# Optimization experiments

Hardware: AMD Instinct MI355X
Metric: run time of the kernel (lower is better)

## Reference

```python
import jax, jax.numpy as jnp
import numpy as np

B, L, CIN, DLOI, NPTS0, NPTS1, H = 2, 5000, 256, 128, 32, 8, 256
HALF = DLOI // 2
EPS = 1e-5


def _bn_params(k, c):
    k1, k2, k3, k4 = jax.random.split(k, 4)
    gamma = 1.0 + 0.1 * jax.random.normal(k1, (c,), jnp.float32)
    beta = 0.1 * jax.random.normal(k2, (c,), jnp.float32)
    mean = 0.1 * jax.random.normal(k3, (c,), jnp.float32)
    var = 0.5 + jax.random.uniform(k4, (c,), jnp.float32)
    return jnp.stack([gamma, beta, mean, var])  # [4, c]


def setup_inputs():
    key = jax.random.key(0)
    ks = jax.random.split(key, 12)
    feature = jax.random.normal(ks[0], (B, CIN, H, H), jnp.float32)
    lines = jax.random.uniform(ks[1], (B, L, 2, 2), jnp.float32, minval=0.0, maxval=255.0)
    w_fc1 = 0.05 * jax.random.normal(ks[2], (DLOI, CIN), jnp.float32)
    b_fc1 = jnp.zeros((DLOI,), jnp.float32)
    bn1 = _bn_params(ks[3], DLOI)
    c1_w = 0.1 * jax.random.normal(ks[4], (HALF, DLOI), jnp.float32)
    c1_b = jnp.zeros((HALF,), jnp.float32)
    bn2 = _bn_params(ks[5], HALF)
    c2_w = 0.1 * jax.random.normal(ks[6], (HALF, HALF, 3), jnp.float32)
    c2_b = jnp.zeros((HALF,), jnp.float32)
    bn3 = _bn_params(ks[7], HALF)
    c3_w = 0.1 * jax.random.normal(ks[8], (DLOI, HALF), jnp.float32)
    c3_b = jnp.zeros((DLOI,), jnp.float32)
    w_fc2 = 0.03 * jax.random.normal(ks[9], (4, DLOI * NPTS1), jnp.float32)
    b_fc2 = jnp.zeros((4,), jnp.float32)
    return {"feature": feature, "lines": lines, "w_fc1": w_fc1, "b_fc1": b_fc1,
            "bn1": bn1, "c1_w": c1_w, "c1_b": c1_b, "bn2": bn2, "c2_w": c2_w,
            "c2_b": c2_b, "bn3": bn3, "c3_w": c3_w, "c3_b": c3_b,
            "w_fc2": w_fc2, "b_fc2": b_fc2}


def _bn(v, p):
    # v: [N, C, P], p: [4, C] = gamma, beta, running_mean, running_var (eval mode)
    scale = (p[0] * jax.lax.rsqrt(p[3] + EPS))[None, :, None]
    shift = p[1][None, :, None]
    return (v - p[2][None, :, None]) * scale + shift


def _forward(feature, lines, w_fc1, b_fc1, bn1, c1_w, c1_b, bn2, c2_w, c2_b,
             bn3, c3_w, c3_b, w_fc2, b_fc2):
    # fc1: 1x1 conv over backbone feature -> [B, DLOI, H, H]
    x = jnp.einsum('bchw,oc->bohw', feature, w_fc1) + b_fc1[None, :, None, None]

    # sample NPTS0 points along each line: p = p0*lam + p1*(1-lam) - 0.5
    lam = jnp.linspace(0.0, 1.0, NPTS0, dtype=jnp.float32)[:, None]  # [NPTS0, 1]
    p = lines[:, :, 0:1, :] * lam + lines[:, :, 1:2, :] * (1.0 - lam) - 0.5  # [B,L,NPTS0,2]
    px, py = p[..., 0], p[..., 1]
    px0 = jnp.clip(jnp.floor(px), 0.0, H - 1.0)
    py0 = jnp.clip(jnp.floor(py), 0.0, H - 1.0)
    px1 = jnp.clip(px0 + 1.0, 0.0, H - 1.0)
    py1 = jnp.clip(py0 + 1.0, 0.0, H - 1.0)
    i0, j0 = px0.astype(jnp.int32), py0.astype(jnp.int32)
    i1, j1 = px1.astype(jnp.int32), py1.astype(jnp.int32)
    w00 = (px1 - px) * (py1 - py)
    w10 = (px - px0) * (py1 - py)
    w01 = (px1 - px) * (py - py0)
    w11 = (px - px0) * (py - py0)

    def gather_one(feat, i0b, j0b, i1b, j1b, a, b, c, d):
        # feat [C,H,W]; indices/weights [L, NPTS0] -> [C, L, NPTS0]
        return (feat[:, i0b, j0b] * a + feat[:, i1b, j0b] * b
                + feat[:, i0b, j1b] * c + feat[:, i1b, j1b] * d)

    xp = jax.vmap(gather_one)(x, i0, j0, i1, j1, w00, w10, w01, w11)  # [B,C,L,NPTS0]
    xp = xp.transpose(0, 2, 1, 3).reshape(B * L, DLOI, NPTS0)

    # MaxPool1d(kernel=4, stride=4): NPTS0 -> NPTS1
    xp = xp.reshape(B * L, DLOI, NPTS1, NPTS0 // NPTS1).max(-1)

    # Bottleneck1D (eval-mode BN): x + op(x)
    h = jax.nn.relu(_bn(xp, bn1))
    h = jnp.einsum('ncp,oc->nop', h, c1_w) + c1_b[None, :, None]
    h = jax.nn.relu(_bn(h, bn2))
    h = jax.lax.conv_general_dilated(h, c2_w, window_strides=(1,), padding=((1, 1),),
                                     dimension_numbers=('NCH', 'OIH', 'NCH')) + c2_b[None, :, None]
    h = jax.nn.relu(_bn(h, bn3))
    h = jnp.einsum('ncp,oc->nop', h, c3_w) + c3_b[None, :, None]
    y = xp + h

    # fc2: ReLU + Linear(DLOI*NPTS1 -> 4), then softmax scores
    flat = y.reshape(B * L, DLOI * NPTS1)
    logits = jax.nn.relu(flat) @ w_fc2.T + b_fc2
    s = jax.nn.softmax(logits, axis=-1)
    return s


def reference(feature, lines, w_fc1, b_fc1, bn1, c1_w, c1_b, bn2, c2_w, c2_b,
              bn3, c3_w, c3_b, w_fc2, b_fc2):
    return _forward(feature, lines, w_fc1, b_fc1, bn1, c1_w, c1_b, bn2, c2_w,
                    c2_b, bn3, c3_w, c3_b, w_fc2, b_fc2)
```

## Files before the change

### kernel.cpp

```cpp
#include <hip/hip_runtime.h>
#include <math.h>
#include <stdint.h>

#define HH 256
#define LPB 5000

typedef _Float16 h2v  __attribute__((ext_vector_type(2)));
typedef _Float16 f16x8 __attribute__((ext_vector_type(8)));
typedef float    f32x4 __attribute__((ext_vector_type(4)));

__device__ __forceinline__ h2v u2h(unsigned int u) { return __builtin_bit_cast(h2v, u); }
__device__ __forceinline__ unsigned int h2u(h2v h) { return __builtin_bit_cast(unsigned int, h); }

__device__ __forceinline__ float fdot2(h2v a, unsigned int w, float c) {
#if __has_builtin(__builtin_amdgcn_fdot2)
    return __builtin_amdgcn_fdot2(a, u2h(w), c, false);
#else
    h2v b = u2h(w);
    return c + (float)a[0] * (float)b[0] + (float)a[1] * (float)b[1];
#endif
}

__device__ __forceinline__ h2v relu2(h2v a) {
    h2v z = (h2v)(_Float16)0.f;
#if __has_builtin(__builtin_elementwise_max)
    return __builtin_elementwise_max(a, z);
#else
    h2v r; r[0] = a[0] > z[0] ? a[0] : z[0]; r[1] = a[1] > z[1] ? a[1] : z[1]; return r;
#endif
}
__device__ __forceinline__ h2v hmax2v(h2v a, h2v b) {
#if __has_builtin(__builtin_elementwise_max)
    return __builtin_elementwise_max(a, b);
#else
    h2v r; r[0] = a[0] > b[0] ? a[0] : b[0]; r[1] = a[1] > b[1] ? a[1] : b[1]; return r;
#endif
}

__global__ __launch_bounds__(256) void prep_small(
    const float* __restrict__ w_fc1, const float* __restrict__ c1w,
    const float* __restrict__ c2w,  const float* __restrict__ c3w,
    const float* __restrict__ wfc2, const float* __restrict__ bn1,
    const float* __restrict__ bn2,  const float* __restrict__ bn3,
    _Float16* __restrict__ wf16, _Float16* __restrict__ w1r,
    _Float16* __restrict__ w2r, _Float16* __restrict__ w3r,
    unsigned int* __restrict__ wfc2p, unsigned int* __restrict__ bn_pk)
{
    int i = blockIdx.x * 256 + threadIdx.x;
    if (i < 32768) { wf16[i] = (_Float16)w_fc1[i]; return; }
    i -= 32768;
    if (i < 8192) {
        w1r[i] = (_Float16)c1w[i]; return;
    }
    i -= 8192;
    if (i < 12288) {
        int ii = i & 63, o = (i >> 6) & 63, tap = i >> 12;
        w2r[i] = (_Float16)c2w[(o * 64 + ii) * 3 + tap]; return;
    }
    i -= 12288;
    if (i < 8192) {
        w3r[i] = (_Float16)c3w[i]; return;
    }
    i -= 8192;
    if (i < 2048) {
        int c2 = i & 63, p = (i >> 6) & 7, j = i >> 9;
        h2v v = { (_Float16)wfc2[j * 1024 + (2 * c2) * 8 + p],
                  (_Float16)wfc2[j * 1024 + (2 * c2 + 1) * 8 + p] };
        wfc2p[(j * 8 + p) * 64 + c2] = h2u(v); return;
    }
    i -= 2048;
    if (i < 128) {
        const float* bn; int C, base, hcount;
        if (i < 64)      { bn = bn1; C = 128; base = 0;   hcount = 64; }
        else if (i < 96) { bn = bn2; C = 64;  base = 128; hcount = 32; i -= 64; }
        else             { bn = bn3; C = 64;  base = 192; hcount = 32; i -= 96; }
        int c0 = 2 * i, c1 = 2 * i + 1;
        float s0 = bn[c0] * rsqrtf(bn[3 * C + c0] + 1e-5f);
        float s1 = bn[c1] * rsqrtf(bn[3 * C + c1] + 1e-5f);
        float h0 = bn[C + c0] - bn[2 * C + c0] * s0;
        float h1 = bn[C + c1] - bn[2 * C + c1] * s1;
        h2v sv = { (_Float16)s0, (_Float16)s1 };
        h2v hv = { (_Float16)h0, (_Float16)h1 };
        bn_pk[base + i] = h2u(sv);
        bn_pk[base + hcount + i] = h2u(hv);
    }
}

__global__ __launch_bounds__(256, 4) void fc1_fused(
    const float* __restrict__ feat,
    const _Float16* __restrict__ W,
    const float* __restrict__ bias,
    unsigned int* __restrict__ X)
{
    __shared__ float Tf[32 * 132];
    __shared__ _Float16 Wl[128 * 40];
    const int t = threadIdx.x;
    const int lane = t & 63, wave = t >> 6;
    const int wm = wave & 1, wn = wave >> 1;
    const int pix0g = blockIdx.x << 7;
    const int b = blockIdx.x >> 9;
    const int pix0l = pix0g & 65535;
    const float* fbase = feat + (size_t)b * (256u * 65536u) + pix0l;

    f32x4 acc[4][4];
#pragma unroll
    for (int a = 0; a < 4; a++)
#pragma unroll
        for (int c = 0; c < 4; c++) acc[a][c] = (f32x4)0.f;

    for (int ks = 0; ks < 8; ks++) {
        const int k0 = ks * 32;
        __syncthreads();
#pragma unroll
        for (int r = 0; r < 4; r++) {
            int idx = t + r * 256;
            int c = idx >> 5, p4 = idx & 31;
            float4 v = *(const float4*)(fbase + (size_t)(k0 + c) * 65536 + p4 * 4);
            *(float4*)&Tf[c * 132 + p4 * 4] = v;
        }
#pragma unroll
        for (int r = 0; r < 2; r++) {
            int idx = t + r * 256;
            int row = idx >> 2, ko = (idx & 3) * 8;
            *(uint4*)&Wl[row * 40 + ko] = *(const uint4*)(W + row * 256 + k0 + ko);
        }
        __syncthreads();
        f16x8 af[4], bf[4];
#pragma unroll
        for (int mt = 0; mt < 4; mt++)
            af[mt] = *(const f16x8*)&Wl[(wm * 64 + mt * 16 + (lane & 15)) * 40 + (lane >> 4) * 8];
#pragma unroll
        for (int nt = 0; nt < 4; nt++) {
            int q = wn * 64 + nt * 16 + (lane & 15);
            int cb = (lane >> 4) * 8;
            f16x8 v;
#pragma unroll
            for (int j = 0; j < 8; j++) v[j] = (_Float16)Tf[(cb + j) * 132 + q];
            bf[nt] = v;
        }
#pragma unroll
        for (int mt = 0; mt < 4; mt++)
#pragma unroll
            for (int nt = 0; nt < 4; nt++)
                acc[mt][nt] = __builtin_amdgcn_mfma_f32_16x16x32_f16(af[mt], bf[nt], acc[mt][nt], 0, 0, 0);
    }
#pragma unroll
    for (int mt = 0; mt < 4; mt++) {
        int o = wm * 64 + mt * 16 + (lane >> 4) * 4;
        float4 b4 = *(const float4*)(bias + o);
#pragma unroll
        for (int nt = 0; nt < 4; nt++) {
            int pix = pix0g + wn * 64 + nt * 16 + (lane & 15);
            f32x4 a = acc[mt][nt];
            h2v lo = { (_Float16)(a[0] + b4.x), (_Float16)(a[1] + b4.y) };
            h2v hi = { (_Float16)(a[2] + b4.z), (_Float16)(a[3] + b4.w) };
            uint2 v = { h2u(lo), h2u(hi) };
            *(uint2*)(X + (size_t)pix * 64 + (o >> 1)) = v;
        }
    }
}

__global__ __launch_bounds__(256, 4) void line_v5(
    const unsigned int* __restrict__ X,
    const float* __restrict__ lines,
    const _Float16* __restrict__ w1r, const float* __restrict__ c1b,
    const _Float16* __restrict__ w2r, const float* __restrict__ c2b,
    const _Float16* __restrict__ w3r, const float* __restrict__ c3b,
    const unsigned int* __restrict__ wfc2p, const float* __restrict__ bfc2,
    const unsigned int* __restrict__ bn_pk,
    float* __restrict__ out)
{
    __shared__ int geoB[256];
    __shared__ unsigned int geoWA[256], geoWB[256];
    __shared__ unsigned int xp[64 * 68];
    __shared__ unsigned int abuf[64 * 68];
    __shared__ float red[128];

    const int t = threadIdx.x;
    const int n0 = blockIdx.x * 8;
    const int lane = t & 63;
    const int w = t >> 6;
    const int l15 = lane & 15;
    const int kg = lane >> 4;
    const int ko8 = kg * 8;

    {
        int l = t >> 5, k = t & 31;
        int n = n0 + l;
        float4 ln = *(const float4*)(lines + n * 4);
        float lam = (float)k / 31.0f;
        float px = ln.x * lam + ln.z * (1.f - lam) - 0.5f;
        float py = ln.y * lam + ln.w * (1.f - lam) - 0.5f;
        float px0 = fminf(fmaxf(floorf(px), 0.f), 255.f);
        float py0 = fminf(fmaxf(floorf(py), 0.f), 255.f);
        float dx = px - px0, dy = py - py0;
        float ex = 1.f - dx, ey = 1.f - dy;
        h2v wA = { (_Float16)(ex * ey), (_Float16)(dx * ey) };
        h2v wB = { (_Float16)(ex * dy), (_Float16)(dx * dy) };
        int b = (n >= LPB) ? 1 : 0;
        int pixflat = (b << 16) + ((int)px0 << 8) + (int)py0;
        geoB[t] = pixflat << 6;
        geoWA[t] = h2u(wA); geoWB[t] = h2u(wB);
    }
    __syncthreads();

    {
        const int c8 = t & 15;
        const int sub = t >> 4;
        const int line = sub >> 1;
        const int gbase = (sub & 1) * 4;
        const uint4* xq = (const uint4*)X;
        uint4 s1 = *(const uint4*)(bn_pk + c8 * 4);
        uint4 h1 = *(const uint4*)(bn_pk + 64 + c8 * 4);
#pragma unroll
        for (int lg = 0; lg < 4; lg++) {
            int g = gbase + lg;
            int ptb = line * 32 + g * 4;
            uint4 q[4][4];
            unsigned int wAv[4], wBv[4];
#pragma unroll
            for (int s = 0; s < 4; s++) {
                int pt = ptb + s;
                int base4 = (geoB[pt] >> 2) + c8;
                wAv[s] = geoWA[pt]; wBv[s] = geoWB[pt];
                q[s][0] = xq[base4];
                q[s][1] = xq[base4 + 4096];
                q[s][2] = xq[base4 + 16];
                q[s][3] = xq[base4 + 4112];
            }
            h2v m0, m1, m2, m3;
#pragma unroll
            for (int s = 0; s < 4; s++) {
                h2v wA = u2h(wAv[s]), wB = u2h(wBv[s]);
                h2v w00 = { wA[0], wA[0] }, w10 = { wA[1], wA[1] };
                h2v w01 = { wB[0], wB[0] }, w11 = { wB[1], wB[1] };
                h2v v0 = u2h(q[s][0].x) * w00 + u2h(q[s][1].x) * w10 + u2h(q[s][2].x) * w01 + u2h(q[s][3].x) * w11;
                h2v v1 = u2h(q[s][0].y) * w00 + u2h(q[s][1].y) * w10 + u2h(q[s][2].y) * w01 + u2h(q[s][3].y) * w11;
                h2v v2 = u2h(q[s][0].z) * w00 + u2h(q[s][1].z) * w10 + u2h(q[s][2].z) * w01 + u2h(q[s][3].z) * w11;
                h2v v3 = u2h(q[s][0].w) * w00 + u2h(q[s][1].w) * w10 + u2h(q[s][2].w) * w01 + u2h(q[s][3].w) * w11;
                if (s == 0) { m0 = v0; m1 = v1; m2 = v2; m3 = v3; }
                else { m0 = hmax2v(m0, v0); m1 = hmax2v(m1, v1);
                       m2 = hmax2v(m2, v2); m3 = hmax2v(m3, v3); }
            }
            int colw = line * 8 + g;
            uint4 raw = { h2u(m0), h2u(m1), h2u(m2), h2u(m3) };
            *(uint4*)&xp[colw * 68 + c8 * 4] = raw;
            h2v r0 = relu2(m0 * u2h(s1.x) + u2h(h1.x));
            h2v r1 = relu2(m1 * u2h(s1.y) + u2h(h1.y));
            h2v r2 = relu2(m2 * u2h(s1.z) + u2h(h1.z));
            h2v r3 = relu2(m3 * u2h(s1.w) + u2h(h1.w));
            uint4 act = { h2u(r0), h2u(r1), h2u(r2), h2u(r3) };
            *(uint4*)&abuf[colw * 68 + c8 * 4] = act;
        }
    }
    __syncthreads();

    f32x4 acc1[4];
#pragma unroll
    for (int nt = 0; nt < 4; nt++) acc1[nt] = (f32x4)0.f;
    {
        const int o = w * 16 + l15;
        f16x8 af[4];
#pragma unroll
        for (int kt = 0; kt < 4; kt++)
            af[kt] = *(const f16x8*)(w1r + o * 128 + kt * 32 + ko8);
        __builtin_amdgcn_s_setprio(1);
#pragma unroll
        for (int nt = 0; nt < 4; nt++) {
            const int colb = nt * 16 + l15;
#pragma unroll
            for (int kt = 0; kt < 4; kt++) {
                f16x8 bf = *(const f16x8*)&abuf[colb * 68 + kt * 16 + kg * 4];
                acc1[nt] = __builtin_amdgcn_mfma_f32_16x16x32_f16(af[kt], bf, acc1[nt], 0, 0, 0);
            }
        }
        __builtin_amdgcn_s_setprio(0);
    }
    __syncthreads();

    {
        float4 b1 = *(const float4*)(c1b + w * 16 + kg * 4);
        const int o2 = w * 8 + kg * 2;
        h2v sA = u2h(bn_pk[128 + o2]), sB = u2h(bn_pk[128 + o2 + 1]);
        h2v hA = u2h(bn_pk[160 + o2]), hB = u2h(bn_pk[160 + o2 + 1]);
#pragma unroll
        for (int nt = 0; nt < 4; nt++) {
            const int col = nt * 16 + l15;
            const int colp = (col >> 3) * 10 + 1 + (col & 7);
            h2v v0 = { (_Float16)(acc1[nt][0] + b1.x), (_Float16)(acc1[nt][1] + b1.y) };
            h2v v1 = { (_Float16)(acc1[nt][2] + b1.z), (_Float16)(acc1[nt][3] + b1.w) };
            v0 = relu2(v0 * sA + hA);
            v1 = relu2(v1 * sB + hB);
            uint2 u = { h2u(v0), h2u(v1) };
            *(uint2*)&abuf[colp * 36 + o2] = u;
        }
#pragma unroll
        for (int e = 0; e < 2; e++) {
            int idx = t * 2 + e;
            int pc = idx >> 5, i2 = idx & 31;
            int pl = pc >> 1, side = pc & 1;
            abuf[(pl * 10 + side * 9) * 36 + i2] = 0;
        }
    }
    __syncthreads();

    f32x4 acc2[4];
#pragma unroll
    for (int nt = 0; nt < 4; nt++) acc2[nt] = (f32x4)0.f;
    {
        const int o = w * 16 + l15;
        const int colp0 = (l15 >> 3) * 10 + 1 + (l15 & 7);
        __builtin_amdgcn_s_setprio(1);
#pragma unroll
        for (int tap = 0; tap < 3; tap++) {
            f16x8 wa0 = *(const f16x8*)(w2r + (tap * 64 + o) * 64 + ko8);
            f16x8 wa1 = *(const f16x8*)(w2r + (tap * 64 + o) * 64 + 32 + ko8);
#pragma unroll
            for (int nt = 0; nt < 4; nt++) {
                const int cp = colp0 + nt * 20 + tap - 1;
                f16x8 b0 = *(const f16x8*)&abuf[cp * 36 + kg * 4];
                f16x8 b1 = *(const f16x8*)&abuf[cp * 36 + 16 + kg * 4];
                acc2[nt] = __builtin_amdgcn_mfma_f32_16x16x32_f16(wa0, b0, acc2[nt], 0, 0, 0);
                acc2[nt] = __builtin_amdgcn_mfma_f32_16x16x32_f16(wa1, b1, acc2[nt], 0, 0, 0);
            }
        }
        __builtin_amdgcn_s_setprio(0);
    }
    __syncthreads();

    {
        float4 b2 = *(const float4*)(c2b + w * 16 + kg * 4);
        const int o2 = w * 8 + kg * 2;
        h2v sA = u2h(bn_pk[192 + o2]), sB = u2h(bn_pk[192 + o2 + 1]);
        h2v hA = u2h(bn_pk[224 + o2]), hB = u2h(bn_pk[224 + o2 + 1]);
#pragma unroll
        for (int nt = 0; nt < 4; nt++) {
            const int col = nt * 16 + l15;
            h2v v0 = { (_Float16)(acc2[nt][0] + b2.x), (_Float16)(acc2[nt][1] + b2.y) };
            h2v v1 = { (_Float16)(acc2[nt][2] + b2.z), (_Float16)(acc2[nt][3] + b2.w) };
            v0 = relu2(v0 * sA + hA);
            v1 = relu2(v1 * sB + hB);
            uint2 u = { h2u(v0), h2u(v1) };
            *(uint2*)&abuf[col * 36 + o2] = u;
        }
    }
    __syncthreads();

    {
#pragma unroll
        for (int mi = 0; mi < 2; mi++) {
            const int om = (2 * w + mi) * 16 + l15;
            f16x8 af0 = *(const f16x8*)(w3r + om * 64 + ko8);
            f16x8 af1 = *(const f16x8*)(w3r + om * 64 + 32 + ko8);
            f32x4 acc3[4];
#pragma unroll
            for (int nt = 0; nt < 4; nt++) acc3[nt] = (f32x4)0.f;
            __builtin_amdgcn_s_setprio(1);
#pragma unroll
            for (int nt = 0; nt < 4; nt++) {
                const int col = nt * 16 + l15;
                f16x8 b0 = *(const f16x8*)&abuf[col * 36 + kg * 4];
                f16x8 b1 = *(const f16x8*)&abuf[col * 36 + 16 + kg * 4];
                acc3[nt] = __builtin_amdgcn_mfma_f32_16x16x32_f16(af0, b0, acc3[nt], 0, 0, 0);
                acc3[nt] = __builtin_amdgcn_mfma_f32_16x16x32_f16(af1, b1, acc3[nt], 0, 0, 0);
            }
            __builtin_amdgcn_s_setprio(0);
            float4 b3 = *(const float4*)(c3b + (2 * w + mi) * 16 + kg * 4);
            const int o2 = (2 * w + mi) * 8 + kg * 2;
#pragma unroll
            for (int nt = 0; nt < 4; nt++) {
                const int col = nt * 16 + l15;
                uint2 xv = *(const uint2*)&xp[col * 68 + o2];
                h2v y0 = { (_Float16)(acc3[nt][0] + b3.x), (_Float16)(acc3[nt][1] + b3.y) };
                h2v y1 = { (_Float16)(acc3[nt][2] + b3.z), (_Float16)(acc3[nt][3] + b3.w) };
                y0 = relu2(u2h(xv.x) + y0);
                y1 = relu2(u2h(xv.y) + y1);
                uint2 u = { h2u(y0), h2u(y1) };
                *(uint2*)&xp[col * 68 + o2] = u;
            }
        }
    }
    __syncthreads();

    {
        const int og = w;
        const int col = t & 63;
        const int obH = __builtin_amdgcn_readfirstlane(og * 16);
        const int p = col & 7, l = col >> 3;
        h2v yv[16];
#pragma unroll
        for (int j = 0; j < 16; j++) yv[j] = u2h(xp[col * 68 + obH + j]);
        float aj[4] = { 0.f, 0.f, 0.f, 0.f };
#pragma unroll
        for (int j = 0; j < 4; j++) {
            unsigned int wv2[16];
#pragma unroll
            for (int q = 0; q < 4; q++)
                *(uint4*)&wv2[q * 4] = *(const uint4*)(wfc2p + (j * 8 + p) * 64 + obH + q * 4);
#pragma unroll
            for (int j16 = 0; j16 < 16; j16++) aj[j] = fdot2(yv[j16], wv2[j16], aj[j]);
        }
#pragma unroll
        for (int off = 4; off > 0; off >>= 1) {
#pragma unroll
            for (int j = 0; j < 4; j++) aj[j] += __shfl_down(aj[j], off, 8);
        }
        if ((t & 7) == 0) {
#pragma unroll
            for (int j = 0; j < 4; j++) red[og * 32 + l * 4 + j] = aj[j];
        }
    }
    __syncthreads();

    if (t < 8) {
        float lg[4];
#pragma unroll
        for (int j = 0; j < 4; j++)
            lg[j] = bfc2[j] + red[t * 4 + j] + red[32 + t * 4 + j]
                  + red[64 + t * 4 + j] + red[96 + t * 4 + j];
        float mx = fmaxf(fmaxf(lg[0], lg[1]), fmaxf(lg[2], lg[3]));
        float e0 = expf(lg[0] - mx), e1 = expf(lg[1] - mx);
        float e2 = expf(lg[2] - mx), e3 = expf(lg[3] - mx);
        float s = 1.f / (e0 + e1 + e2 + e3);
        float4 r = { e0 * s, e1 * s, e2 * s, e3 * s };
        *(float4*)(out + (size_t)(n0 + t) * 4) = r;
    }
}

extern "C" void kernel_launch(void* const* d_in, const int* in_sizes, int n_in,
                              void* d_out, int out_size, void* d_ws, size_t ws_size,
                              hipStream_t stream) {
    const float* feature = (const float*)d_in[0];
    const float* lines   = (const float*)d_in[1];
    const float* w_fc1   = (const float*)d_in[2];
    const float* b_fc1   = (const float*)d_in[3];
    const float* bn1     = (const float*)d_in[4];
    const float* c1_w    = (const float*)d_in[5];
    const float* c1_b    = (const float*)d_in[6];
    const float* bn2     = (const float*)d_in[7];
    const float* c2_w    = (const float*)d_in[8];
    const float* c2_b    = (const float*)d_in[9];
    const float* bn3     = (const float*)d_in[10];
    const float* c3_w    = (const float*)d_in[11];
    const float* c3_b    = (const float*)d_in[12];
    const float* w_fc2   = (const float*)d_in[13];
    const float* b_fc2   = (const float*)d_in[14];
    float* out = (float*)d_out;

    char* ws = (char*)d_ws;
    unsigned int* X     = (unsigned int*)ws;
    _Float16*     wf16  = (_Float16*)(ws + 33554432);
    _Float16*     w1r   = (_Float16*)(ws + 33619968);
    _Float16*     w2r   = (_Float16*)(ws + 33636352);
    _Float16*     w3r   = (_Float16*)(ws + 33660928);
    unsigned int* wfc2p = (unsigned int*)(ws + 33677312);
    unsigned int* bn_pk = (unsigned int*)(ws + 33685504);

    prep_small<<<249, 256, 0, stream>>>(w_fc1, c1_w, c2_w, c3_w, w_fc2, bn1, bn2, bn3,
                                        wf16, w1r, w2r, w3r, wfc2p, bn_pk);
    fc1_fused<<<1024, 256, 0, stream>>>(feature, wf16, b_fc1, X);
    line_v5<<<1250, 256, 0, stream>>>(X, lines, w1r, c1_b, w2r, c2_b,
                                      w3r, c3_b, wfc2p, b_fc2, bn_pk, out);
}
```

Measured before the change: 269.4 us.

## Sort lines spatially by midpoint bucket and remap blocks per XCD for locality

Adds a counting-sort pass, run in an extra block of the prep kernel, that buckets lines by batch and the 16x16 tile holding their midpoint. The line kernel then processes lines in that sorted order and writes each result back to its original index. Block IDs are also remapped so each XCD handles a contiguous range of sorted lines, so nearby samples of X share the per-XCD L2. The costs are a serial prefix scan in one block, an extra indirection load, and scattered output writes.

After: 294.3 us. 1.09x slower.

```diff
diff --git a/kernel.cpp b/kernel.cpp
--- a/kernel.cpp
+++ b/kernel.cpp
@@ -42,10 +42,43 @@
     const float* __restrict__ c2w,  const float* __restrict__ c3w,
     const float* __restrict__ wfc2, const float* __restrict__ bn1,
     const float* __restrict__ bn2,  const float* __restrict__ bn3,
+    const float* __restrict__ lines,
     _Float16* __restrict__ wf16, _Float16* __restrict__ w1r,
     _Float16* __restrict__ w2r, _Float16* __restrict__ w3r,
-    unsigned int* __restrict__ wfc2p, unsigned int* __restrict__ bn_pk)
+    unsigned int* __restrict__ wfc2p, unsigned int* __restrict__ bn_pk,
+    int* __restrict__ perm)
 {
+    if (blockIdx.x == 249) {
+        __shared__ int cnt[512];
+        __shared__ int base[512];
+        const int t = threadIdx.x;
+        for (int j = t; j < 512; j += 256) cnt[j] = 0;
+        __syncthreads();
+        for (int i = t; i < 10000; i += 256) {
+            float4 ln = *(const float4*)(lines + i * 4);
+            float mx = 0.5f * (ln.x + ln.z), my = 0.5f * (ln.y + ln.w);
+            int bx = min(max((int)mx, 0), 255) >> 4;
+            int by = min(max((int)my, 0), 255) >> 4;
+            int bk = ((i >= LPB) ? 256 : 0) + by * 16 + bx;
+            atomicAdd(&cnt[bk], 1);
+        }
+        __syncthreads();
+        if (t == 0) {
+            int s = 0;
+            for (int j = 0; j < 512; j++) { base[j] = s; s += cnt[j]; }
+        }
+        __syncthreads();
+        for (int i = t; i < 10000; i += 256) {
+            float4 ln = *(const float4*)(lines + i * 4);
+            float mx = 0.5f * (ln.x + ln.z), my = 0.5f * (ln.y + ln.w);
+            int bx = min(max((int)mx, 0), 255) >> 4;
+            int by = min(max((int)my, 0), 255) >> 4;
+            int bk = ((i >= LPB) ? 256 : 0) + by * 16 + bx;
+            int rank = atomicAdd(&base[bk], 1);
+            perm[rank] = i;
+        }
+        return;
+    }
     int i = blockIdx.x * 256 + threadIdx.x;
     if (i < 32768) { wf16[i] = (_Float16)w_fc1[i]; return; }
     i -= 32768;
@@ -70,10 +103,10 @@
     }
     i -= 2048;
     if (i < 128) {
-        const float* bn; int C, base, hcount;
-        if (i < 64)      { bn = bn1; C = 128; base = 0;   hcount = 64; }
-        else if (i < 96) { bn = bn2; C = 64;  base = 128; hcount = 32; i -= 64; }
-        else             { bn = bn3; C = 64;  base = 192; hcount = 32; i -= 96; }
+        const float* bn; int C, base_, hcount;
+        if (i < 64)      { bn = bn1; C = 128; base_ = 0;   hcount = 64; }
+        else if (i < 96) { bn = bn2; C = 64;  base_ = 128; hcount = 32; i -= 64; }
+        else             { bn = bn3; C = 64;  base_ = 192; hcount = 32; i -= 96; }
         int c0 = 2 * i, c1 = 2 * i + 1;
         float s0 = bn[c0] * rsqrtf(bn[3 * C + c0] + 1e-5f);
         float s1 = bn[c1] * rsqrtf(bn[3 * C + c1] + 1e-5f);
@@ -81,8 +114,8 @@
         float h1 = bn[C + c1] - bn[2 * C + c1] * s1;
         h2v sv = { (_Float16)s0, (_Float16)s1 };
         h2v hv = { (_Float16)h0, (_Float16)h1 };
-        bn_pk[base + i] = h2u(sv);
-        bn_pk[base + hcount + i] = h2u(hv);
+        bn_pk[base_ + i] = h2u(sv);
+        bn_pk[base_ + hcount + i] = h2u(hv);
     }
 }
 
@@ -160,9 +193,10 @@
     }
 }
 
-__global__ __launch_bounds__(256, 4) void line_v5(
+__global__ __launch_bounds__(256, 4) void line_v6(
     const unsigned int* __restrict__ X,
     const float* __restrict__ lines,
+    const int* __restrict__ perm,
     const _Float16* __restrict__ w1r, const float* __restrict__ c1b,
     const _Float16* __restrict__ w2r, const float* __restrict__ c2b,
     const _Float16* __restrict__ w3r, const float* __restrict__ c3b,
@@ -177,7 +211,10 @@
     __shared__ float red[128];
 
     const int t = threadIdx.x;
-    const int n0 = blockIdx.x * 8;
+    const int orig = blockIdx.x;
+    const int xcd = orig & 7, loc = orig >> 3;
+    const int bid = (xcd < 2 ? xcd * 157 : 2 * 157 + (xcd - 2) * 156) + loc;
+    const int n0 = bid * 8;
     const int lane = t & 63;
     const int w = t >> 6;
     const int l15 = lane & 15;
@@ -186,8 +223,8 @@
 
     {
         int l = t >> 5, k = t & 31;
-        int n = n0 + l;
-        float4 ln = *(const float4*)(lines + n * 4);
+        int id = perm[n0 + l];
+        float4 ln = *(const float4*)(lines + id * 4);
         float lam = (float)k / 31.0f;
         float px = ln.x * lam + ln.z * (1.f - lam) - 0.5f;
         float py = ln.y * lam + ln.w * (1.f - lam) - 0.5f;
@@ -197,7 +234,7 @@
         float ex = 1.f - dx, ey = 1.f - dy;
         h2v wA = { (_Float16)(ex * ey), (_Float16)(dx * ey) };
         h2v wB = { (_Float16)(ex * dy), (_Float16)(dx * dy) };
-        int b = (n >= LPB) ? 1 : 0;
+        int b = (id >= LPB) ? 1 : 0;
         int pixflat = (b << 16) + ((int)px0 << 8) + (int)py0;
         geoB[t] = pixflat << 6;
         geoWA[t] = h2u(wA); geoWB[t] = h2u(wB);
@@ -413,6 +450,7 @@
     __syncthreads();
 
     if (t < 8) {
+        int id = perm[n0 + t];
         float lg[4];
 #pragma unroll
         for (int j = 0; j < 4; j++)
@@ -423,7 +461,7 @@
         float e2 = expf(lg[2] - mx), e3 = expf(lg[3] - mx);
         float s = 1.f / (e0 + e1 + e2 + e3);
         float4 r = { e0 * s, e1 * s, e2 * s, e3 * s };
-        *(float4*)(out + (size_t)(n0 + t) * 4) = r;
+        *(float4*)(out + (size_t)id * 4) = r;
     }
 }
 
@@ -455,10 +493,11 @@
     _Float16*     w3r   = (_Float16*)(ws + 33660928);
     unsigned int* wfc2p = (unsigned int*)(ws + 33677312);
     unsigned int* bn_pk = (unsigned int*)(ws + 33685504);
-
-    prep_small<<<249, 256, 0, stream>>>(w_fc1, c1_w, c2_w, c3_w, w_fc2, bn1, bn2, bn3,
-                                        wf16, w1r, w2r, w3r, wfc2p, bn_pk);
+    int*          perm  = (int*)(ws + 33686528);
+
+    prep_small<<<250, 256, 0, stream>>>(w_fc1, c1_w, c2_w, c3_w, w_fc2, bn1, bn2, bn3,
+                                        lines, wf16, w1r, w2r, w3r, wfc2p, bn_pk, perm);
     fc1_fused<<<1024, 256, 0, stream>>>(feature, wf16, b_fc1, X);
-    line_v5<<<1250, 256, 0, stream>>>(X, lines, w1r, c1_b, w2r, c2_b,
+    line_v6<<<1250, 256, 0, stream>>>(X, lines, perm, w1r, c1_b, w2r, c2_b,
                                       w3r, c3_b, wfc2p, b_fc2, bn_pk, out);
 }
```
